# Kernel tuning notes

Measured on AMD Instinct MI355X. Metric: run time of the kernel, lower is better.

Reference implementation:

```python
import jax, jax.numpy as jnp
import numpy as np

D_MODEL = 768
NUM_HEADS = 12
D_HEAD = D_MODEL // NUM_HEADS


def setup_inputs() -> dict:
    key = jax.random.key(0)
    ks = jax.random.split(key, 11)
    B, S = 1, 4096
    s = 1.0 / np.sqrt(D_MODEL)
    inp = {
        'q': jax.random.normal(ks[0], (B, S, D_MODEL), dtype=jnp.float32),
        'k': jax.random.normal(ks[1], (B, S, D_MODEL), dtype=jnp.float32),
        'v': jax.random.normal(ks[2], (B, S, D_MODEL), dtype=jnp.float32),
        'wq': jax.random.normal(ks[3], (D_MODEL, D_MODEL), dtype=jnp.float32) * s,
        'bq': jnp.zeros((D_MODEL,), dtype=jnp.float32),
        'wk': jax.random.normal(ks[4], (D_MODEL, D_MODEL), dtype=jnp.float32) * s,
        'bk': jnp.zeros((D_MODEL,), dtype=jnp.float32),
        'wv': jax.random.normal(ks[5], (D_MODEL, D_MODEL), dtype=jnp.float32) * s,
        'bv': jnp.zeros((D_MODEL,), dtype=jnp.float32),
        'wo': jax.random.normal(ks[6], (D_MODEL, D_MODEL), dtype=jnp.float32) * s,
        'bo': jnp.zeros((D_MODEL,), dtype=jnp.float32),
    }
    return inp


def reference(q, k, v, wq, bq, wk, bk, wv, bv, wo, bo):
    B, S, _ = q.shape
    # linear projections (torch Linear: x @ W^T + b)
    qh = (q @ wq.T + bq).reshape(B, S, NUM_HEADS, D_HEAD).transpose(0, 2, 1, 3)
    kh = (k @ wk.T + bk).reshape(B, S, NUM_HEADS, D_HEAD).transpose(0, 2, 1, 3)
    vh = (v @ wv.T + bv).reshape(B, S, NUM_HEADS, D_HEAD).transpose(0, 2, 1, 3)
    scores = jnp.einsum('bhqd,bhkd->bhqk', qh, kh) / jnp.sqrt(jnp.float32(D_HEAD))
    causal = jnp.tril(jnp.ones((S, S), dtype=bool))  # [S,S] causal mask
    scores = jnp.where(causal, scores, jnp.finfo(scores.dtype).min)
    attn = jax.nn.softmax(scores, axis=-1)  # dropout omitted (eval mode)
    out = jnp.einsum('bhqk,bhkd->bhqd', attn, vh)
    out = out.transpose(0, 2, 1, 3).reshape(B, S, D_MODEL)
    return out @ wo.T + bo
```

## Files before the change

### kernel.cpp

```cpp
#include <hip/hip_runtime.h>
#include <stdint.h>

typedef __attribute__((ext_vector_type(8))) short short8;
typedef __attribute__((ext_vector_type(4))) float float4v;
typedef __attribute__((ext_vector_type(2))) uint32_t uint32x2;
typedef __attribute__((ext_vector_type(4))) uint32_t uint32x4;

__device__ __forceinline__ unsigned short f2bf(float f) {
  union { float f; uint32_t u; } v;
  v.f = f;
  uint32_t u = v.u;
  return (unsigned short)((u + 0x7fffu + ((u >> 16) & 1u)) >> 16);
}

__device__ __forceinline__ uint32_t pkbf(float a, float b) {
#if __has_builtin(__builtin_amdgcn_cvt_pk_bf16_f32)
  typedef __attribute__((ext_vector_type(2))) __bf16 bf16x2;
  bf16x2 r = __builtin_amdgcn_cvt_pk_bf16_f32(a, b);
  union { bf16x2 v; uint32_t u; } c;
  c.v = r;
  return c.u;
#else
  return (uint32_t)f2bf(a) | ((uint32_t)f2bf(b) << 16);
#endif
}

__device__ __forceinline__ float fexp2(float x) {
#if __has_builtin(__builtin_amdgcn_exp2f)
  return __builtin_amdgcn_exp2f(x);
#else
  return exp2f(x);
#endif
}

__device__ __forceinline__ void gll16(const unsigned short* g, unsigned short* l) {
  __builtin_amdgcn_global_load_lds(
      (const __attribute__((address_space(1))) void*)g,
      (__attribute__((address_space(3))) void*)l, 16, 0, 0);
}

struct CvtArgs {
  const float* src[7];
  unsigned short* dst[7];
};

__global__ __launch_bounds__(256) void cvt_all(CvtArgs a) {
  const int bid = blockIdx.x;
  int t, off;
  if (bid < 4608) { t = bid / 1536; off = bid - t * 1536; }
  else { const int b2 = bid - 4608; t = 3 + b2 / 288; off = b2 - (t - 3) * 288; }
  const size_t i = (size_t)off * 256 + threadIdx.x;
  const float4v* p = (const float4v*)(a.src[t] + i * 8);
  float4v x = p[0], y = p[1];
  uint32x4 o;
  o[0] = pkbf(x[0], x[1]);
  o[1] = pkbf(x[2], x[3]);
  o[2] = pkbf(y[0], y[1]);
  o[3] = pkbf(y[2], y[3]);
  *(uint32x4*)(a.dst[t] + i * 8) = o;
}

__global__ __launch_bounds__(256) void gemm_qkv(
    const unsigned short* __restrict__ xq, const unsigned short* __restrict__ xk,
    const unsigned short* __restrict__ xv,
    const unsigned short* __restrict__ wqb, const unsigned short* __restrict__ wkb,
    const unsigned short* __restrict__ wvb,
    const float* __restrict__ bq, const float* __restrict__ bk,
    const float* __restrict__ bv,
    unsigned short* __restrict__ Qp, unsigned short* __restrict__ Kp,
    unsigned short* __restrict__ Vt, float qscale)
{
  __shared__ unsigned short As[128 * 64];
  __shared__ unsigned short Ws[128 * 64];
  const int z = blockIdx.z;
  const unsigned short* A = z == 0 ? xq : z == 1 ? xk : xv;
  const unsigned short* W = z == 0 ? wqb : z == 1 ? wkb : wvb;
  const float* bias = z == 0 ? bq : z == 1 ? bk : bv;
  const int M = 4096, N = 768, K = 768;
  const int tid = threadIdx.x, wave = tid >> 6, lane = tid & 63;
  const int g = lane >> 4, l16 = lane & 15;
  const int sw = l16 & 7;
  const int m0 = blockIdx.x * 128, n0 = blockIdx.y * 128;
  const int wn = (wave >> 1) * 64, wm = (wave & 1) * 64;
  const int srow0 = wave * 32 + (lane >> 3);
  const int skg = lane & 7;

  float4v acc[4][4] = {};

  for (int k0 = 0; k0 < K; k0 += 64) {
    if (k0) __syncthreads();
    #pragma unroll
    for (int c = 0; c < 4; ++c) {
      const int row = srow0 + c * 8;
      const int kg = skg ^ (row & 7);
      gll16(A + (size_t)(m0 + row) * K + k0 + kg * 8, &As[(wave * 32 + c * 8) * 64]);
      gll16(W + (size_t)(n0 + row) * K + k0 + kg * 8, &Ws[(wave * 32 + c * 8) * 64]);
    }
    __syncthreads();
    #pragma unroll
    for (int kk = 0; kk < 2; ++kk) {
      const int kg = ((kk * 4 + g) ^ sw) * 8;
      short8 xf[4], wf[4];
      #pragma unroll
      for (int t = 0; t < 4; ++t) {
        xf[t] = *(const short8*)&As[(wm + t * 16 + l16) * 64 + kg];
        wf[t] = *(const short8*)&Ws[(wn + t * 16 + l16) * 64 + kg];
      }
      if (z < 2) {
        #pragma unroll
        for (int i = 0; i < 4; ++i)
          #pragma unroll
          for (int j = 0; j < 4; ++j)
            acc[i][j] = __builtin_amdgcn_mfma_f32_16x16x32_bf16(wf[i], xf[j], acc[i][j], 0, 0, 0);
      } else {
        #pragma unroll
        for (int i = 0; i < 4; ++i)
          #pragma unroll
          for (int j = 0; j < 4; ++j)
            acc[i][j] = __builtin_amdgcn_mfma_f32_16x16x32_bf16(xf[i], wf[j], acc[i][j], 0, 0, 0);
      }
    }
  }

  if (z < 2) {
    unsigned short* O = z == 0 ? Qp : Kp;
    const float osc = z == 0 ? qscale : 1.0f;
    #pragma unroll
    for (int i = 0; i < 4; ++i) {
      const int nb = n0 + wn + i * 16 + 4 * g;
      const float4v bb = *(const float4v*)&bias[nb];
      #pragma unroll
      for (int j = 0; j < 4; ++j) {
        const int m = m0 + wm + j * 16 + l16;
        uint32x2 pk;
        pk[0] = pkbf((acc[i][j][0] + bb[0]) * osc, (acc[i][j][1] + bb[1]) * osc);
        pk[1] = pkbf((acc[i][j][2] + bb[2]) * osc, (acc[i][j][3] + bb[3]) * osc);
        *(uint32x2*)(O + (size_t)m * N + nb) = pk;
      }
    }
  } else {
    #pragma unroll
    for (int j = 0; j < 4; ++j) {
      const int n = n0 + wn + j * 16 + l16;
      const float bb = bias[n];
      #pragma unroll
      for (int i = 0; i < 4; ++i) {
        const int mb = m0 + wm + i * 16 + 4 * g;
        uint32x2 pk;
        pk[0] = pkbf(acc[i][j][0] + bb, acc[i][j][1] + bb);
        pk[1] = pkbf(acc[i][j][2] + bb, acc[i][j][3] + bb);
        *(uint32x2*)(Vt + (size_t)n * M + mb) = pk;
      }
    }
  }
}

__global__ __launch_bounds__(256, 2) void flash_attn(
    const unsigned short* __restrict__ Qp,
    const unsigned short* __restrict__ Kp,
    const unsigned short* __restrict__ Vt,
    unsigned short* __restrict__ AO)
{
  __shared__ unsigned short lds_k[2][64 * 64];
  __shared__ unsigned short lds_v[2][64 * 64];
  __shared__ unsigned short lds_p[4][32 * 64];
  const int S = 4096, DM = 768;

  const int gid = blockIdx.x;
  const int x = gid & 7, r = gid >> 3;
  const bool heavy = r < 24;
  const int p = x * 24 + (heavy ? r : r - 24);
  const int h = p >> 4, tp = p & 15;
  const int qtile = heavy ? 31 - tp : tp;

  const int tid = threadIdx.x, wave = tid >> 6, lane = tid & 63;
  const int g = lane >> 4, l16 = lane & 15;
  const int sw = l16 & 7;
  const int qbase = qtile * 128 + wave * 32;

  short8 qf[2][2];
  #pragma unroll
  for (int qc = 0; qc < 2; ++qc) {
    const unsigned short* qp = Qp + (size_t)(qbase + qc * 16 + l16) * DM + h * 64;
    qf[qc][0] = *(const short8*)(qp + g * 8);
    qf[qc][1] = *(const short8*)(qp + 32 + g * 8);
  }

  float4v o[2][4] = {};
  float lsum[2] = {0.0f, 0.0f};

  const int strow = wave * 16 + (lane >> 3);
  const int skg = lane & 7;

  #pragma unroll
  for (int c = 0; c < 2; ++c) {
    const int row = strow + c * 8;
    const int kg = skg ^ (row & 7);
    gll16(Kp + (size_t)row * DM + h * 64 + kg * 8, &lds_k[0][(wave * 16 + c * 8) * 64]);
    gll16(Vt + (size_t)(h * 64 + row) * S + kg * 8, &lds_v[0][(wave * 16 + c * 8) * 64]);
  }
  __syncthreads();

  const int kmax = 2 * qtile + 1;
  for (int kb = 0; kb <= kmax; ++kb) {
    const int cur = kb & 1;
    if (kb < kmax) {
      const int nb = cur ^ 1;
      #pragma unroll
      for (int c = 0; c < 2; ++c) {
        const int row = strow + c * 8;
        const int kg = skg ^ (row & 7);
        gll16(Kp + (size_t)((kb + 1) * 64 + row) * DM + h * 64 + kg * 8,
              &lds_k[nb][(wave * 16 + c * 8) * 64]);
        gll16(Vt + (size_t)(h * 64 + row) * S + (kb + 1) * 64 + kg * 8,
              &lds_v[nb][(wave * 16 + c * 8) * 64]);
      }
    }
    const unsigned short* kc = lds_k[cur];
    const unsigned short* vc = lds_v[cur];

    float4v sf[2][4];
    #pragma unroll
    for (int mt = 0; mt < 4; ++mt) {
      short8 ka0 = *(const short8*)&kc[(mt * 16 + l16) * 64 + ((0 + g) ^ sw) * 8];
      short8 ka1 = *(const short8*)&kc[(mt * 16 + l16) * 64 + ((4 + g) ^ sw) * 8];
      #pragma unroll
      for (int qc = 0; qc < 2; ++qc) {
        float4v a = {};
        a = __builtin_amdgcn_mfma_f32_16x16x32_bf16(ka0, qf[qc][0], a, 0, 0, 0);
        a = __builtin_amdgcn_mfma_f32_16x16x32_bf16(ka1, qf[qc][1], a, 0, 0, 0);
        sf[qc][mt] = a;
      }
    }

    if ((kb + 1) * 64 > qbase) {
      #pragma unroll
      for (int qc = 0; qc < 2; ++qc) {
        const int q = qbase + qc * 16 + l16;
        #pragma unroll
        for (int mt = 0; mt < 4; ++mt)
          #pragma unroll
          for (int rr = 0; rr < 4; ++rr) {
            const int key = kb * 64 + mt * 16 + 4 * g + rr;
            sf[qc][mt][rr] = (key <= q) ? sf[qc][mt][rr] : -1e30f;
          }
      }
    }

    #pragma unroll
    for (int qc = 0; qc < 2; ++qc)
      #pragma unroll
      for (int mt = 0; mt < 4; ++mt)
        #pragma unroll
        for (int rr = 0; rr < 4; ++rr) {
          const float pe = fexp2(sf[qc][mt][rr]);
          sf[qc][mt][rr] = pe;
          lsum[qc] += pe;
        }

    unsigned short* pw = lds_p[wave];
    #pragma unroll
    for (int qc = 0; qc < 2; ++qc) {
      #pragma unroll
      for (int mt = 0; mt < 4; ++mt) {
        uint32x2 pp;
        pp[0] = pkbf(sf[qc][mt][0], sf[qc][mt][1]);
        pp[1] = pkbf(sf[qc][mt][2], sf[qc][mt][3]);
        const int kgp = mt * 2 + (g >> 1);
        *(uint32x2*)&pw[(qc * 16 + l16) * 64 + ((kgp ^ sw) * 8) + (g & 1) * 4] = pp;
      }
    }
    __builtin_amdgcn_wave_barrier();

    #pragma unroll
    for (int ks2 = 0; ks2 < 2; ++ks2) {
      short8 pf[2];
      #pragma unroll
      for (int qc = 0; qc < 2; ++qc)
        pf[qc] = *(const short8*)&pw[(qc * 16 + l16) * 64 + (((ks2 * 4 + g) ^ sw) * 8)];
      #pragma unroll
      for (int dt = 0; dt < 4; ++dt) {
        short8 va = *(const short8*)&vc[(dt * 16 + l16) * 64 + (((ks2 * 4 + g) ^ sw) * 8)];
        #pragma unroll
        for (int qc = 0; qc < 2; ++qc)
          o[qc][dt] = __builtin_amdgcn_mfma_f32_16x16x32_bf16(va, pf[qc], o[qc][dt], 0, 0, 0);
      }
    }

    __syncthreads();
  }

  #pragma unroll
  for (int qc = 0; qc < 2; ++qc) {
    float L = lsum[qc];
    L += __shfl_xor(L, 16);
    L += __shfl_xor(L, 32);
    const float inv = 1.0f / L;
    const int q = qbase + qc * 16 + l16;
    #pragma unroll
    for (int dt = 0; dt < 4; ++dt) {
      uint32x2 ov;
      ov[0] = pkbf(o[qc][dt][0] * inv, o[qc][dt][1] * inv);
      ov[1] = pkbf(o[qc][dt][2] * inv, o[qc][dt][3] * inv);
      *(uint32x2*)(AO + (size_t)q * DM + h * 64 + dt * 16 + 4 * g) = ov;
    }
  }
}

__global__ __launch_bounds__(256) void gemm_out(
    const unsigned short* __restrict__ A, const unsigned short* __restrict__ W,
    const float* __restrict__ bias, float* __restrict__ Out)
{
  __shared__ unsigned short As[128 * 64];
  __shared__ unsigned short Ws[128 * 64];
  const int N = 768, K = 768;
  const int tid = threadIdx.x, wave = tid >> 6, lane = tid & 63;
  const int g = lane >> 4, l16 = lane & 15;
  const int sw = l16 & 7;
  const int m0 = blockIdx.x * 128, n0 = blockIdx.y * 128;
  const int wn = (wave >> 1) * 64, wm = (wave & 1) * 64;
  const int srow0 = wave * 32 + (lane >> 3);
  const int skg = lane & 7;

  float4v acc[4][4] = {};

  for (int k0 = 0; k0 < K; k0 += 64) {
    if (k0) __syncthreads();
    #pragma unroll
    for (int c = 0; c < 4; ++c) {
      const int row = srow0 + c * 8;
      const int kg = skg ^ (row & 7);
      gll16(A + (size_t)(m0 + row) * K + k0 + kg * 8, &As[(wave * 32 + c * 8) * 64]);
      gll16(W + (size_t)(n0 + row) * K + k0 + kg * 8, &Ws[(wave * 32 + c * 8) * 64]);
    }
    __syncthreads();
    #pragma unroll
    for (int kk = 0; kk < 2; ++kk) {
      const int kg = ((kk * 4 + g) ^ sw) * 8;
      short8 xf[4], wf[4];
      #pragma unroll
      for (int t = 0; t < 4; ++t) {
        xf[t] = *(const short8*)&As[(wm + t * 16 + l16) * 64 + kg];
        wf[t] = *(const short8*)&Ws[(wn + t * 16 + l16) * 64 + kg];
      }
      #pragma unroll
      for (int i = 0; i < 4; ++i)
        #pragma unroll
        for (int j = 0; j < 4; ++j)
          acc[i][j] = __builtin_amdgcn_mfma_f32_16x16x32_bf16(wf[i], xf[j], acc[i][j], 0, 0, 0);
    }
  }

  #pragma unroll
  for (int i = 0; i < 4; ++i) {
    const int nb = n0 + wn + i * 16 + 4 * g;
    const float4v bb = *(const float4v*)&bias[nb];
    #pragma unroll
    for (int j = 0; j < 4; ++j) {
      const int m = m0 + wm + j * 16 + l16;
      float4v ov;
      #pragma unroll
      for (int rr = 0; rr < 4; ++rr) ov[rr] = acc[i][j][rr] + bb[rr];
      *(float4v*)(Out + (size_t)m * N + nb) = ov;
    }
  }
}

extern "C" void kernel_launch(void* const* d_in, const int* in_sizes, int n_in,
                              void* d_out, int out_size, void* d_ws, size_t ws_size,
                              hipStream_t stream) {
  const float* q  = (const float*)d_in[0];
  const float* k  = (const float*)d_in[1];
  const float* v  = (const float*)d_in[2];
  const float* wq = (const float*)d_in[3];
  const float* bq = (const float*)d_in[4];
  const float* wk = (const float*)d_in[5];
  const float* bk = (const float*)d_in[6];
  const float* wv = (const float*)d_in[7];
  const float* bv = (const float*)d_in[8];
  const float* wo = (const float*)d_in[9];
  const float* bo = (const float*)d_in[10];
  float* out = (float*)d_out;

  const int S = 4096, D = 768;
  unsigned short* Qp  = (unsigned short*)d_ws;
  unsigned short* Kp  = Qp  + (size_t)S * D;
  unsigned short* Vt  = Kp  + (size_t)S * D;
  unsigned short* AO  = Vt  + (size_t)S * D;
  unsigned short* xq  = AO  + (size_t)S * D;
  unsigned short* xk  = xq  + (size_t)S * D;
  unsigned short* xv  = xk  + (size_t)S * D;
  unsigned short* wqb = xv  + (size_t)S * D;
  unsigned short* wkb = wqb + (size_t)D * D;
  unsigned short* wvb = wkb + (size_t)D * D;
  unsigned short* wob = wvb + (size_t)D * D;

  CvtArgs ca;
  ca.src[0] = q;  ca.dst[0] = xq;
  ca.src[1] = k;  ca.dst[1] = xk;
  ca.src[2] = v;  ca.dst[2] = xv;
  ca.src[3] = wq; ca.dst[3] = wqb;
  ca.src[4] = wk; ca.dst[4] = wkb;
  ca.src[5] = wv; ca.dst[5] = wvb;
  ca.src[6] = wo; ca.dst[6] = wob;

  const float SC = 0.125f * 1.44269504089f;
  dim3 blk(256);
  cvt_all<<<dim3(5760), blk, 0, stream>>>(ca);
  gemm_qkv<<<dim3(32, 6, 3), blk, 0, stream>>>(xq, xk, xv, wqb, wkb, wvb,
                                               bq, bk, bv, Qp, Kp, Vt, SC);
  flash_attn<<<dim3(384), blk, 0, stream>>>(Qp, Kp, Vt, AO);
  gemm_out<<<dim3(32, 6), blk, 0, stream>>>(AO, wob, bo, out);
}
```

Measured before the change: 235.2 us.

## Split causal attention over KV chunks and add a combine kernel

The single flash-attention kernel becomes a split-KV version. Each block handles one query tile for up to 16 KV blocks and writes unnormalized bf16 partial outputs plus row sums to workspace. A new combine kernel sums the partials and normalizes them. The block index is mapped so heavy tiles are scheduled first, and launch bounds are raised to 3 blocks per CU. The aim is to balance the causal workload across more blocks and CUs, at the cost of an extra launch, extra workspace traffic and bf16 rounding of the partials.

```diff
diff --git a/kernel.cpp b/kernel.cpp
--- a/kernel.cpp
+++ b/kernel.cpp
@@ -155,11 +155,12 @@
   }
 }
 
-__global__ __launch_bounds__(256, 2) void flash_attn(
+__global__ __launch_bounds__(256, 3) void flash_part(
     const unsigned short* __restrict__ Qp,
     const unsigned short* __restrict__ Kp,
     const unsigned short* __restrict__ Vt,
-    unsigned short* __restrict__ AO)
+    unsigned short* __restrict__ Opart,
+    float* __restrict__ lpart)
 {
   __shared__ unsigned short lds_k[2][64 * 64];
   __shared__ unsigned short lds_v[2][64 * 64];
@@ -167,16 +168,20 @@
   const int S = 4096, DM = 768;
 
   const int gid = blockIdx.x;
-  const int x = gid & 7, r = gid >> 3;
-  const bool heavy = r < 24;
-  const int p = x * 24 + (heavy ? r : r - 24);
-  const int h = p >> 4, tp = p & 15;
-  const int qtile = heavy ? 31 - tp : tp;
+  const int h = gid % 12;
+  const int e = 79 - gid / 12;
+  int t, c;
+  if (e < 8)       { t = e;                c = 0; }
+  else if (e < 24) { t = 8 + (e - 8) / 2;  c = (e - 8) % 2; }
+  else if (e < 48) { t = 16 + (e - 24) / 3; c = (e - 24) % 3; }
+  else             { t = 24 + (e - 48) / 4; c = (e - 48) % 4; }
+  const int kb0 = c * 16;
+  const int kbe = min(kb0 + 16, 2 * t + 2);
 
   const int tid = threadIdx.x, wave = tid >> 6, lane = tid & 63;
   const int g = lane >> 4, l16 = lane & 15;
   const int sw = l16 & 7;
-  const int qbase = qtile * 128 + wave * 32;
+  const int qbase = t * 128 + wave * 32;
 
   short8 qf[2][2];
   #pragma unroll
@@ -193,27 +198,28 @@
   const int skg = lane & 7;
 
   #pragma unroll
-  for (int c = 0; c < 2; ++c) {
-    const int row = strow + c * 8;
+  for (int cc = 0; cc < 2; ++cc) {
+    const int row = strow + cc * 8;
     const int kg = skg ^ (row & 7);
-    gll16(Kp + (size_t)row * DM + h * 64 + kg * 8, &lds_k[0][(wave * 16 + c * 8) * 64]);
-    gll16(Vt + (size_t)(h * 64 + row) * S + kg * 8, &lds_v[0][(wave * 16 + c * 8) * 64]);
+    gll16(Kp + (size_t)(kb0 * 64 + row) * DM + h * 64 + kg * 8,
+          &lds_k[0][(wave * 16 + cc * 8) * 64]);
+    gll16(Vt + (size_t)(h * 64 + row) * S + kb0 * 64 + kg * 8,
+          &lds_v[0][(wave * 16 + cc * 8) * 64]);
   }
   __syncthreads();
 
-  const int kmax = 2 * qtile + 1;
-  for (int kb = 0; kb <= kmax; ++kb) {
+  for (int kb = kb0; kb < kbe; ++kb) {
     const int cur = kb & 1;
-    if (kb < kmax) {
+    if (kb + 1 < kbe) {
       const int nb = cur ^ 1;
       #pragma unroll
-      for (int c = 0; c < 2; ++c) {
-        const int row = strow + c * 8;
+      for (int cc = 0; cc < 2; ++cc) {
+        const int row = strow + cc * 8;
         const int kg = skg ^ (row & 7);
         gll16(Kp + (size_t)((kb + 1) * 64 + row) * DM + h * 64 + kg * 8,
-              &lds_k[nb][(wave * 16 + c * 8) * 64]);
+              &lds_k[nb][(wave * 16 + cc * 8) * 64]);
         gll16(Vt + (size_t)(h * 64 + row) * S + (kb + 1) * 64 + kg * 8,
-              &lds_v[nb][(wave * 16 + c * 8) * 64]);
+              &lds_v[nb][(wave * 16 + cc * 8) * 64]);
       }
     }
     const unsigned short* kc = lds_k[cur];
@@ -290,20 +296,65 @@
     __syncthreads();
   }
 
+  const int slot = (h * 32 + t) * 4 + c;
+  unsigned short* ob = Opart + (size_t)slot * 8192;
   #pragma unroll
   for (int qc = 0; qc < 2; ++qc) {
     float L = lsum[qc];
     L += __shfl_xor(L, 16);
     L += __shfl_xor(L, 32);
-    const float inv = 1.0f / L;
-    const int q = qbase + qc * 16 + l16;
+    const int ql = wave * 32 + qc * 16 + l16;
+    if (g == 0) lpart[slot * 128 + ql] = L;
     #pragma unroll
     for (int dt = 0; dt < 4; ++dt) {
       uint32x2 ov;
-      ov[0] = pkbf(o[qc][dt][0] * inv, o[qc][dt][1] * inv);
-      ov[1] = pkbf(o[qc][dt][2] * inv, o[qc][dt][3] * inv);
-      *(uint32x2*)(AO + (size_t)q * DM + h * 64 + dt * 16 + 4 * g) = ov;
-    }
+      ov[0] = pkbf(o[qc][dt][0], o[qc][dt][1]);
+      ov[1] = pkbf(o[qc][dt][2], o[qc][dt][3]);
+      *(uint32x2*)(ob + (size_t)ql * 64 + dt * 16 + 4 * g) = ov;
+    }
+  }
+}
+
+__global__ __launch_bounds__(256) void flash_combine(
+    const unsigned short* __restrict__ Opart, const float* __restrict__ lpart,
+    unsigned short* __restrict__ AO)
+{
+  const int t = blockIdx.x, h = blockIdx.y;
+  const int nc = (2 * t + 17) >> 4;
+  const int slot0 = (h * 32 + t) * 4;
+  const int tid = threadIdx.x;
+  const int qr = tid >> 2, dc = (tid & 3) * 16;
+  #pragma unroll
+  for (int it = 0; it < 2; ++it) {
+    const int ql = it * 64 + qr;
+    float acc[16];
+    #pragma unroll
+    for (int j = 0; j < 16; ++j) acc[j] = 0.0f;
+    float lsum = 0.0f;
+    for (int cc = 0; cc < nc; ++cc) {
+      const int slot = slot0 + cc;
+      lsum += lpart[slot * 128 + ql];
+      const uint32x4* p = (const uint32x4*)(Opart + (size_t)slot * 8192 + ql * 64 + dc);
+      uint32x4 w0 = p[0], w1 = p[1];
+      #pragma unroll
+      for (int j = 0; j < 4; ++j) {
+        union { uint32_t u; float f; } lo, hi;
+        lo.u = w0[j] << 16; hi.u = w0[j] & 0xffff0000u;
+        acc[2 * j] += lo.f; acc[2 * j + 1] += hi.f;
+        lo.u = w1[j] << 16; hi.u = w1[j] & 0xffff0000u;
+        acc[8 + 2 * j] += lo.f; acc[8 + 2 * j + 1] += hi.f;
+      }
+    }
+    const float inv = 1.0f / lsum;
+    uint32x4 o0, o1;
+    #pragma unroll
+    for (int j = 0; j < 4; ++j) {
+      o0[j] = pkbf(acc[2 * j] * inv, acc[2 * j + 1] * inv);
+      o1[j] = pkbf(acc[8 + 2 * j] * inv, acc[8 + 2 * j + 1] * inv);
+    }
+    unsigned short* dst = AO + (size_t)(t * 128 + ql) * 768 + h * 64 + dc;
+    *(uint32x4*)dst = o0;
+    *(uint32x4*)(dst + 8) = o1;
   }
 }
 
@@ -383,17 +434,19 @@
   float* out = (float*)d_out;
 
   const int S = 4096, D = 768;
-  unsigned short* Qp  = (unsigned short*)d_ws;
-  unsigned short* Kp  = Qp  + (size_t)S * D;
-  unsigned short* Vt  = Kp  + (size_t)S * D;
-  unsigned short* AO  = Vt  + (size_t)S * D;
-  unsigned short* xq  = AO  + (size_t)S * D;
-  unsigned short* xk  = xq  + (size_t)S * D;
-  unsigned short* xv  = xk  + (size_t)S * D;
-  unsigned short* wqb = xv  + (size_t)S * D;
-  unsigned short* wkb = wqb + (size_t)D * D;
-  unsigned short* wvb = wkb + (size_t)D * D;
-  unsigned short* wob = wvb + (size_t)D * D;
+  unsigned short* Qp    = (unsigned short*)d_ws;
+  unsigned short* Kp    = Qp  + (size_t)S * D;
+  unsigned short* Vt    = Kp  + (size_t)S * D;
+  unsigned short* AO    = Vt  + (size_t)S * D;
+  unsigned short* xq    = AO  + (size_t)S * D;
+  unsigned short* xk    = xq  + (size_t)S * D;
+  unsigned short* xv    = xk  + (size_t)S * D;
+  unsigned short* wqb   = xv  + (size_t)S * D;
+  unsigned short* wkb   = wqb + (size_t)D * D;
+  unsigned short* wvb   = wkb + (size_t)D * D;
+  unsigned short* wob   = wvb + (size_t)D * D;
+  unsigned short* Opart = wob + (size_t)D * D;
+  float*          lpart = (float*)(Opart + (size_t)1536 * 8192);
 
   CvtArgs ca;
   ca.src[0] = q;  ca.dst[0] = xq;
@@ -409,6 +462,7 @@
   cvt_all<<<dim3(5760), blk, 0, stream>>>(ca);
   gemm_qkv<<<dim3(32, 6, 3), blk, 0, stream>>>(xq, xk, xv, wqb, wkb, wvb,
                                                bq, bk, bv, Qp, Kp, Vt, SC);
-  flash_attn<<<dim3(384), blk, 0, stream>>>(Qp, Kp, Vt, AO);
+  flash_part<<<dim3(960), blk, 0, stream>>>(Qp, Kp, Vt, Opart, lpart);
+  flash_combine<<<dim3(32, 12), blk, 0, stream>>>(Opart, lpart, AO);
   gemm_out<<<dim3(32, 6), blk, 0, stream>>>(AO, wob, bo, out);
 }
```

Result: faster. 213.2 us (-9.4%).
